# Kernel optimization log

Measured on AMD Instinct MI355X. Metric: run time of the kernel, lower is better.

Reference implementation:

```python
import jax, jax.numpy as jnp
import numpy as np

HEADS = 8  # head_dim = 512 // 8 = 64


def setup_inputs() -> dict:
    key = jax.random.key(0)
    ks = jax.random.split(key, 6)
    B, S, D = 1, 4096, 512
    s = 0.02
    return {
        "hidden_states": jax.random.normal(ks[0], (B, S, D), dtype=jnp.float32),
        "Wq": jax.random.normal(ks[1], (D, D), dtype=jnp.float32) * s,
        "Wk": jax.random.normal(ks[2], (D, D), dtype=jnp.float32) * s,
        "Wv": jax.random.normal(ks[3], (D, D), dtype=jnp.float32) * s,
        "Wo": jax.random.normal(ks[4], (D, D), dtype=jnp.float32) * s,
        "b_out": jnp.zeros((D,), dtype=jnp.float32),
    }


def reference(hidden_states, Wq, Wk, Wv, Wo, b_out):
    B, S, D = hidden_states.shape
    H = HEADS
    hd = D // H
    scale = 1.0 / jnp.sqrt(jnp.asarray(hd, hidden_states.dtype))

    # unfused QKV projections (self-attention, no mask)
    q = hidden_states @ Wq  # [B,S,D]
    k = hidden_states @ Wk
    v = hidden_states @ Wv

    # head_to_batch_dim: [B,S,D] -> [B,H,S,hd]
    def split_heads(t):
        return t.reshape(B, S, H, hd).transpose(0, 2, 1, 3)

    q, k, v = split_heads(q), split_heads(k), split_heads(v)

    # explicit score matrix + softmax (faithful to torch.bmm path)
    scores = jnp.einsum("bhqd,bhkd->bhqk", q, k) * scale  # [B,H,S,S]
    probs = jax.nn.softmax(scores, axis=-1)
    out = jnp.einsum("bhqk,bhkd->bhqd", probs, v)  # [B,H,S,hd]

    # batch_to_head_dim: [B,H,S,hd] -> [B,S,D]
    out = out.transpose(0, 2, 1, 3).reshape(B, S, D)
    # to_out[0] Linear + to_out[1] Dropout (identity at eval)
    return out @ Wo + b_out
```

## Files before the change

kernel.cpp:

```cpp
#include <hip/hip_runtime.h>
#include <hip/hip_bf16.h>

#define S_LEN 4096
#define DMODEL 512
#define NHEADS 8
#define HDIM 64

typedef __hip_bfloat16 bf16;
typedef __attribute__((ext_vector_type(8))) short bf16x8;
typedef __attribute__((ext_vector_type(4))) float f32x4;
typedef __attribute__((ext_vector_type(4))) _Float16 f16x4;
typedef __attribute__((ext_vector_type(8))) _Float16 f16x8;

__device__ __forceinline__ f32x4 mfma16x16x32(bf16x8 a, bf16x8 b, f32x4 c) {
    return __builtin_amdgcn_mfma_f32_16x16x32_bf16(a, b, c, 0, 0, 0);
}
__device__ __forceinline__ f32x4 mfma16x16x16h(f16x4 a, f16x4 b, f32x4 c) {
    return __builtin_amdgcn_mfma_f32_16x16x16f16(a, b, c, 0, 0, 0);
}
__device__ __forceinline__ f16x4 lo4(f16x8 v) { return __builtin_shufflevector(v, v, 0, 1, 2, 3); }
__device__ __forceinline__ f16x4 hi4(f16x8 v) { return __builtin_shufflevector(v, v, 4, 5, 6, 7); }
__device__ __forceinline__ void gload_lds16(const void* g, void* l) {
    __builtin_amdgcn_global_load_lds(
        (const __attribute__((address_space(1))) unsigned int*)g,
        (__attribute__((address_space(3))) unsigned int*)l, 16, 0, 0);
}

__global__ __launch_bounds__(256) void prep(
    const float* __restrict__ X,
    const float* __restrict__ Wq, const float* __restrict__ Wk,
    const float* __restrict__ Wv, const float* __restrict__ Wo,
    bf16* __restrict__ Xb, bf16* __restrict__ Wt)
{
    __shared__ bf16 tile[32][33];
    const int b = blockIdx.x;
    if (b < 1024) {
        int i = (b * 256 + threadIdx.x) * 8;
        float4 a = *(const float4*)(X + i);
        float4 c = *(const float4*)(X + i + 4);
        bf16 tmp[8];
        tmp[0] = __float2bfloat16(a.x); tmp[1] = __float2bfloat16(a.y);
        tmp[2] = __float2bfloat16(a.z); tmp[3] = __float2bfloat16(a.w);
        tmp[4] = __float2bfloat16(c.x); tmp[5] = __float2bfloat16(c.y);
        tmp[6] = __float2bfloat16(c.z); tmp[7] = __float2bfloat16(c.w);
        *(bf16x8*)(Xb + i) = *(bf16x8*)tmp;
    } else {
        const int bb = b - 1024;
        const int z = bb >> 8;
        const int bx = bb & 15, by = (bb >> 4) & 15;
        const float* src = (z == 0) ? Wq : (z == 1) ? Wk : (z == 2) ? Wv : Wo;
        bf16* dst = Wt + (size_t)z * DMODEL * DMODEL;
        const int tx = threadIdx.x & 31, ty = threadIdx.x >> 5;
        const int x = bx * 32 + tx;
        const int y0 = by * 32;
        #pragma unroll
        for (int i = ty; i < 32; i += 8)
            tile[i][tx] = __float2bfloat16(src[(size_t)(y0 + i) * DMODEL + x]);
        __syncthreads();
        const int xo = y0 + tx;
        #pragma unroll
        for (int i = ty; i < 32; i += 8)
            dst[(size_t)(bx * 32 + i) * DMODEL + xo] = tile[tx][i];
    }
}

__global__ __launch_bounds__(256) void gemm_qkv(
    const bf16* __restrict__ A, const bf16* __restrict__ Bt,
    bf16* __restrict__ Qm, bf16* __restrict__ Km, _Float16* __restrict__ Vt)
{
    __shared__ __align__(16) bf16 As[2][64 * 64];
    __shared__ __align__(16) bf16 Bs[2][64 * 64];
    const int m0 = blockIdx.x * 64, n0 = blockIdx.y * 64;
    const int t = threadIdx.x, lane = t & 63, w = t >> 6;
    const int lr = lane & 15, lq = lane >> 4;
    const int swz = (lr & 7) << 4;

    f32x4 acc[4] = {f32x4{0,0,0,0}, f32x4{0,0,0,0}, f32x4{0,0,0,0}, f32x4{0,0,0,0}};

    const int srow = w * 8 + (lane >> 3);
    const int scol = ((lane & 7) ^ (lane >> 3)) * 8;
    const bf16* Ab = A + (size_t)(m0 + srow) * DMODEL + scol;
    const bf16* Bb = Bt + (size_t)(n0 + srow) * DMODEL + scol;
    const int lb = (w * 8) * 64;

#define QKV_STAGE(k0, bsel) do {                                        \
        gload_lds16(Ab + (k0), &As[bsel][lb]);                          \
        gload_lds16(Ab + 32 * DMODEL + (k0), &As[bsel][lb + 32 * 64]);  \
        gload_lds16(Bb + (k0), &Bs[bsel][lb]);                          \
        gload_lds16(Bb + 32 * DMODEL + (k0), &Bs[bsel][lb + 32 * 64]);  \
    } while (0)

    QKV_STAGE(0, 0);
    #pragma unroll
    for (int ks = 0; ks < 8; ++ks) {
        const int cur = ks & 1;
        if (ks < 7) {
            QKV_STAGE((ks + 1) * 64, cur ^ 1);
            asm volatile("s_waitcnt vmcnt(4)" ::: "memory");
        } else {
            asm volatile("s_waitcnt vmcnt(0)" ::: "memory");
        }
        __builtin_amdgcn_s_barrier();
        __builtin_amdgcn_sched_barrier(0);
        const char* Ab8 = (const char*)&As[cur][0];
        const char* Bb8 = (const char*)&Bs[cur][0];
        #pragma unroll
        for (int kc = 0; kc < 2; ++kc) {
            bf16x8 a = *(const bf16x8*)(Ab8 + (w * 16 + lr) * 128 + ((kc * 64 + lq * 16) ^ swz));
            #pragma unroll
            for (int nt = 0; nt < 4; ++nt) {
                bf16x8 b = *(const bf16x8*)(Bb8 + (nt * 16 + lr) * 128 + ((kc * 64 + lq * 16) ^ swz));
                acc[nt] = mfma16x16x32(a, b, acc[nt]);
            }
        }
        asm volatile("s_waitcnt lgkmcnt(0)" ::: "memory");
        __builtin_amdgcn_sched_barrier(0);
        __builtin_amdgcn_s_barrier();
    }
#undef QKV_STAGE

    const int which = n0 >> 9;
    const int nloc = n0 & 511;
    if (which == 0) {
        #pragma unroll
        for (int nt = 0; nt < 4; ++nt)
            #pragma unroll
            for (int r = 0; r < 4; ++r)
                Qm[(size_t)(m0 + w * 16 + lq * 4 + r) * DMODEL + nloc + nt * 16 + lr] =
                    __float2bfloat16(acc[nt][r] * 0.18033688f);
    } else if (which == 1) {
        #pragma unroll
        for (int nt = 0; nt < 4; ++nt)
            #pragma unroll
            for (int r = 0; r < 4; ++r)
                Km[(size_t)(m0 + w * 16 + lq * 4 + r) * DMODEL + nloc + nt * 16 + lr] =
                    __float2bfloat16(acc[nt][r]);
    } else {
        _Float16* tb = (_Float16*)As;
        #pragma unroll
        for (int nt = 0; nt < 4; ++nt)
            #pragma unroll
            for (int r = 0; r < 4; ++r)
                tb[(w * 16 + lq * 4 + r) * 72 + nt * 16 + lr] = (_Float16)acc[nt][r];
        __syncthreads();
        const int c = t >> 2, seg = t & 3;
        _Float16 tmp[16];
        #pragma unroll
        for (int j = 0; j < 16; ++j)
            tmp[j] = tb[(seg * 16 + j) * 72 + c];
        _Float16* vp = Vt + (size_t)(nloc + c) * S_LEN + m0;
        #pragma unroll
        for (int g = 0; g < 4; ++g) {
            f16x4 vv = {tmp[g * 4 + 0], tmp[g * 4 + 1], tmp[g * 4 + 2], tmp[g * 4 + 3]};
            *(f16x4*)(vp + g * 16 + seg * 4) = vv;
        }
    }
}

__global__ __launch_bounds__(256) void gemm_out(
    const bf16* __restrict__ A, const bf16* __restrict__ Bt,
    float* __restrict__ Out, const float* __restrict__ bias)
{
    __shared__ __align__(16) bf16 As[2][64 * 64];
    __shared__ __align__(16) bf16 Bs[2][64 * 64];
    const int m0 = blockIdx.x * 64, n0 = blockIdx.y * 64;
    const int t = threadIdx.x, lane = t & 63, w = t >> 6;
    const int lr = lane & 15, lq = lane >> 4;
    const int swz = (lr & 7) << 4;

    f32x4 acc[4] = {f32x4{0,0,0,0}, f32x4{0,0,0,0}, f32x4{0,0,0,0}, f32x4{0,0,0,0}};

    const int srow = w * 8 + (lane >> 3);
    const int scol = ((lane & 7) ^ (lane >> 3)) * 8;
    const bf16* Ab = A + (size_t)(m0 + srow) * DMODEL + scol;
    const bf16* Bb = Bt + (size_t)(n0 + srow) * DMODEL + scol;
    const int lb = (w * 8) * 64;

#define OUT_STAGE(k0, bsel) do {                                        \
        gload_lds16(Ab + (k0), &As[bsel][lb]);                          \
        gload_lds16(Ab + 32 * DMODEL + (k0), &As[bsel][lb + 32 * 64]);  \
        gload_lds16(Bb + (k0), &Bs[bsel][lb]);                          \
        gload_lds16(Bb + 32 * DMODEL + (k0), &Bs[bsel][lb + 32 * 64]);  \
    } while (0)

    OUT_STAGE(0, 0);
    #pragma unroll
    for (int ks = 0; ks < 8; ++ks) {
        const int cur = ks & 1;
        if (ks < 7) {
            OUT_STAGE((ks + 1) * 64, cur ^ 1);
            asm volatile("s_waitcnt vmcnt(4)" ::: "memory");
        } else {
            asm volatile("s_waitcnt vmcnt(0)" ::: "memory");
        }
        __builtin_amdgcn_s_barrier();
        __builtin_amdgcn_sched_barrier(0);
        const char* Ab8 = (const char*)&As[cur][0];
        const char* Bb8 = (const char*)&Bs[cur][0];
        #pragma unroll
        for (int kc = 0; kc < 2; ++kc) {
            bf16x8 a = *(const bf16x8*)(Ab8 + (w * 16 + lr) * 128 + ((kc * 64 + lq * 16) ^ swz));
            #pragma unroll
            for (int nt = 0; nt < 4; ++nt) {
                bf16x8 b = *(const bf16x8*)(Bb8 + (nt * 16 + lr) * 128 + ((kc * 64 + lq * 16) ^ swz));
                acc[nt] = mfma16x16x32(a, b, acc[nt]);
            }
        }
        asm volatile("s_waitcnt lgkmcnt(0)" ::: "memory");
        __builtin_amdgcn_sched_barrier(0);
        __builtin_amdgcn_s_barrier();
    }
#undef OUT_STAGE

    #pragma unroll
    for (int nt = 0; nt < 4; ++nt)
        #pragma unroll
        for (int r = 0; r < 4; ++r)
            Out[(size_t)(m0 + w * 16 + lq * 4 + r) * DMODEL + n0 + nt * 16 + lr] =
                acc[nt][r] + bias[n0 + nt * 16 + lr];
}

__global__ __launch_bounds__(256, 2) void attn_kernel(
    const bf16* __restrict__ Q, const bf16* __restrict__ Kmat,
    const _Float16* __restrict__ Vt, bf16* __restrict__ Oout)
{
    __shared__ __align__(16) char smem[65536];

    const int h = blockIdx.x, qb = blockIdx.y;
    const int t = threadIdx.x, lane = t & 63, w = t >> 6;
    const int lr = lane & 15, lq = lane >> 4;
    const int q0 = qb * 64;

    char* myK = smem + w * 16384;
    char* myV = myK + 8192;

    const int sr = lane >> 3;
    const int scc = (lane & 7) ^ sr;
    const bf16*     gK = Kmat + (size_t)sr * DMODEL + h * HDIM + scc * 8;
    const _Float16* gV = Vt + (size_t)(h * HDIM + sr) * S_LEN + scc * 8;

    bf16x8 qf[4][2];
    #pragma unroll
    for (int qt = 0; qt < 4; ++qt) {
        const bf16* qp = Q + (size_t)(q0 + qt * 16 + lr) * DMODEL + h * HDIM + lq * 8;
        qf[qt][0] = *(const bf16x8*)qp;
        qf[qt][1] = *(const bf16x8*)(qp + 32);
    }

    f32x4 oacc[4][4];
    #pragma unroll
    for (int i = 0; i < 4; ++i)
        #pragma unroll
        for (int j = 0; j < 4; ++j) oacc[i][j] = f32x4{0, 0, 0, 0};
    float lsum[4] = {0, 0, 0, 0};

    #pragma unroll
    for (int i = 0; i < 8; ++i) {
        gload_lds16(gK + (size_t)(w * 64 + i * 8) * DMODEL, myK + i * 1024);
        gload_lds16(gV + (size_t)(i * 8) * S_LEN + w * 64, myV + i * 1024);
    }

    const int swz = (lr & 7) << 4;

    for (int kt = w; kt < S_LEN / 64; kt += 4) {
        asm volatile("s_waitcnt vmcnt(0)" ::: "memory");

        bf16x8 kf[4][2];
        #pragma unroll
        for (int mt = 0; mt < 4; ++mt) {
            const char* kr = myK + (mt * 16 + lr) * 128;
            kf[mt][0] = *(const bf16x8*)(kr + ((lq * 16) ^ swz));
            kf[mt][1] = *(const bf16x8*)(kr + ((64 + lq * 16) ^ swz));
        }
        f16x8 vA[4], vB[4];
        #pragma unroll
        for (int ht = 0; ht < 4; ++ht) {
            const char* vr = myV + (ht * 16 + lr) * 128;
            vA[ht] = *(const f16x8*)(vr + ((lq * 32) ^ swz));
            vB[ht] = *(const f16x8*)(vr + ((lq * 32 + 16) ^ swz));
        }
        asm volatile("s_waitcnt lgkmcnt(0)" ::: "memory");
        __builtin_amdgcn_sched_barrier(0);

        const int ktn = kt + 4;
        if (ktn < S_LEN / 64) {
            #pragma unroll
            for (int i = 0; i < 8; ++i) {
                gload_lds16(gK + (size_t)(ktn * 64 + i * 8) * DMODEL, myK + i * 1024);
                gload_lds16(gV + (size_t)(i * 8) * S_LEN + ktn * 64, myV + i * 1024);
            }
        }

        __builtin_amdgcn_s_setprio(1);
        f16x4 pf[4][4];
        #pragma unroll
        for (int qt = 0; qt < 4; ++qt) {
            f32x4 st[4];
            #pragma unroll
            for (int mt = 0; mt < 4; ++mt) {
                f32x4 z = {0, 0, 0, 0};
                z = mfma16x16x32(kf[mt][0], qf[qt][0], z);
                z = mfma16x16x32(kf[mt][1], qf[qt][1], z);
                st[mt] = z;
            }
            #pragma unroll
            for (int mt = 0; mt < 4; ++mt)
                #pragma unroll
                for (int r = 0; r < 4; ++r) {
                    float p = __builtin_amdgcn_exp2f(st[mt][r]);
                    lsum[qt] += p;
                    pf[qt][mt][r] = (_Float16)p;
                }
        }
        #pragma unroll
        for (int qt = 0; qt < 4; ++qt)
            #pragma unroll
            for (int ht = 0; ht < 4; ++ht) {
                oacc[qt][ht] = mfma16x16x16h(pf[qt][0], lo4(vA[ht]), oacc[qt][ht]);
                oacc[qt][ht] = mfma16x16x16h(pf[qt][1], hi4(vA[ht]), oacc[qt][ht]);
                oacc[qt][ht] = mfma16x16x16h(pf[qt][2], lo4(vB[ht]), oacc[qt][ht]);
                oacc[qt][ht] = mfma16x16x16h(pf[qt][3], hi4(vB[ht]), oacc[qt][ht]);
            }
        __builtin_amdgcn_s_setprio(0);
    }

    __syncthreads();
    float (*obuf)[3][4][64][4] = (float(*)[3][4][64][4])smem;
    float (*lbuf)[4][16]       = (float(*)[4][16])(smem + 49152);

    #pragma unroll
    for (int qt = 0; qt < 4; ++qt) {
        if (qt != w) {
            int j = qt - (qt > w ? 1 : 0);
            #pragma unroll
            for (int ht = 0; ht < 4; ++ht)
                *(f32x4*)&obuf[w][j][ht][lane][0] = oacc[qt][ht];
        }
    }
    #pragma unroll
    for (int qt = 0; qt < 4; ++qt) {
        float s = lsum[qt];
        s += __shfl_xor(s, 16);
        s += __shfl_xor(s, 32);
        if (lq == 0) lbuf[w][qt][lr] = s;
    }
    __syncthreads();

    f32x4 osum[4];
    #pragma unroll
    for (int qt = 0; qt < 4; ++qt)
        if (qt == w) {
            #pragma unroll
            for (int ht = 0; ht < 4; ++ht) osum[ht] = oacc[qt][ht];
        }
    #pragma unroll
    for (int w2 = 0; w2 < 4; ++w2) {
        if (w2 == w) continue;
        int j = w - (w > w2 ? 1 : 0);
        #pragma unroll
        for (int ht = 0; ht < 4; ++ht)
            osum[ht] += *(const f32x4*)&obuf[w2][j][ht][lane][0];
    }
    float linv[4];
    #pragma unroll
    for (int r = 0; r < 4; ++r) {
        int rr = lq * 4 + r;
        linv[r] = 1.0f / (lbuf[0][w][rr] + lbuf[1][w][rr] + lbuf[2][w][rr] + lbuf[3][w][rr]);
    }
    #pragma unroll
    for (int r = 0; r < 4; ++r) {
        int row = q0 + w * 16 + lq * 4 + r;
        #pragma unroll
        for (int ht = 0; ht < 4; ++ht)
            Oout[(size_t)row * DMODEL + h * HDIM + ht * 16 + lr] =
                __float2bfloat16(osum[ht][r] * linv[r]);
    }
}

extern "C" void kernel_launch(void* const* d_in, const int* in_sizes, int n_in,
                              void* d_out, int out_size, void* d_ws, size_t ws_size,
                              hipStream_t stream) {
    const float* X  = (const float*)d_in[0];
    const float* Wq = (const float*)d_in[1];
    const float* Wk = (const float*)d_in[2];
    const float* Wv = (const float*)d_in[3];
    const float* Wo = (const float*)d_in[4];
    const float* bo = (const float*)d_in[5];
    float* out = (float*)d_out;

    char* ws = (char*)d_ws;
    bf16* Wt = (bf16*)ws;
    bf16* Xb = (bf16*)(ws + (size_t)4 * DMODEL * DMODEL * 2);
    bf16* Qm = Xb + (size_t)S_LEN * DMODEL;
    bf16* Km = Qm + (size_t)S_LEN * DMODEL;
    _Float16* Vt = (_Float16*)(Km + (size_t)S_LEN * DMODEL);
    bf16* AO = (bf16*)(Vt + (size_t)S_LEN * DMODEL);

    bf16* Wot = Wt + (size_t)3 * DMODEL * DMODEL;

    prep<<<2048, 256, 0, stream>>>(X, Wq, Wk, Wv, Wo, Xb, Wt);

    gemm_qkv<<<dim3(S_LEN / 64, 3 * DMODEL / 64), 256, 0, stream>>>(
        Xb, Wt, Qm, Km, Vt);

    attn_kernel<<<dim3(NHEADS, S_LEN / 64), 256, 0, stream>>>(Qm, Km, Vt, AO);

    gemm_out<<<dim3(S_LEN / 64, DMODEL / 64), 256, 0, stream>>>(AO, Wot, out, bo);
}
```

Baseline: 134.7 us.

## Fuse QKV tiles per block, use 16x16x32 f16 MFMA, vectorize epilogues

The QKV GEMM now computes Q, K and V tiles for the same rows in one block, reusing the A tile across three weight matrices and cutting the grid to a third. Epilogues for Q/K and the output GEMM are staged through shared memory so global stores become 16-byte row-contiguous writes. In attention, the four 16x16x16 f16 MFMAs per tile are replaced by two 16x16x32 f16 MFMAs, and probabilities are packed with cvt_pkrtz conversions. The trade-offs are more LDS per QKV block (64KB) with lower occupancy, and round-toward-zero rounding of the probabilities.

```diff
diff --git a/kernel.cpp b/kernel.cpp
--- a/kernel.cpp
+++ b/kernel.cpp
@@ -9,17 +9,16 @@
 typedef __hip_bfloat16 bf16;
 typedef __attribute__((ext_vector_type(8))) short bf16x8;
 typedef __attribute__((ext_vector_type(4))) float f32x4;
+typedef __attribute__((ext_vector_type(2))) _Float16 f16x2;
 typedef __attribute__((ext_vector_type(4))) _Float16 f16x4;
 typedef __attribute__((ext_vector_type(8))) _Float16 f16x8;
 
 __device__ __forceinline__ f32x4 mfma16x16x32(bf16x8 a, bf16x8 b, f32x4 c) {
     return __builtin_amdgcn_mfma_f32_16x16x32_bf16(a, b, c, 0, 0, 0);
 }
-__device__ __forceinline__ f32x4 mfma16x16x16h(f16x4 a, f16x4 b, f32x4 c) {
-    return __builtin_amdgcn_mfma_f32_16x16x16f16(a, b, c, 0, 0, 0);
-}
-__device__ __forceinline__ f16x4 lo4(f16x8 v) { return __builtin_shufflevector(v, v, 0, 1, 2, 3); }
-__device__ __forceinline__ f16x4 hi4(f16x8 v) { return __builtin_shufflevector(v, v, 4, 5, 6, 7); }
+__device__ __forceinline__ f32x4 mfma16x16x32h(f16x8 a, f16x8 b, f32x4 c) {
+    return __builtin_amdgcn_mfma_f32_16x16x32_f16(a, b, c, 0, 0, 0);
+}
 __device__ __forceinline__ void gload_lds16(const void* g, void* l) {
     __builtin_amdgcn_global_load_lds(
         (const __attribute__((address_space(1))) unsigned int*)g,
@@ -68,26 +67,33 @@
     const bf16* __restrict__ A, const bf16* __restrict__ Bt,
     bf16* __restrict__ Qm, bf16* __restrict__ Km, _Float16* __restrict__ Vt)
 {
-    __shared__ __align__(16) bf16 As[2][64 * 64];
-    __shared__ __align__(16) bf16 Bs[2][64 * 64];
+    __shared__ __align__(16) char smem[65536];
     const int m0 = blockIdx.x * 64, n0 = blockIdx.y * 64;
     const int t = threadIdx.x, lane = t & 63, w = t >> 6;
     const int lr = lane & 15, lq = lane >> 4;
     const int swz = (lr & 7) << 4;
 
-    f32x4 acc[4] = {f32x4{0,0,0,0}, f32x4{0,0,0,0}, f32x4{0,0,0,0}, f32x4{0,0,0,0}};
+    f32x4 acc[3][4];
+    #pragma unroll
+    for (int i = 0; i < 3; ++i)
+        #pragma unroll
+        for (int n = 0; n < 4; ++n) acc[i][n] = f32x4{0, 0, 0, 0};
 
     const int srow = w * 8 + (lane >> 3);
     const int scol = ((lane & 7) ^ (lane >> 3)) * 8;
     const bf16* Ab = A + (size_t)(m0 + srow) * DMODEL + scol;
     const bf16* Bb = Bt + (size_t)(n0 + srow) * DMODEL + scol;
-    const int lb = (w * 8) * 64;
-
-#define QKV_STAGE(k0, bsel) do {                                        \
-        gload_lds16(Ab + (k0), &As[bsel][lb]);                          \
-        gload_lds16(Ab + 32 * DMODEL + (k0), &As[bsel][lb + 32 * 64]);  \
-        gload_lds16(Bb + (k0), &Bs[bsel][lb]);                          \
-        gload_lds16(Bb + 32 * DMODEL + (k0), &Bs[bsel][lb + 32 * 64]);  \
+
+#define QKV_STAGE(k0, b) do {                                                  \
+        char* ad = smem + (b) * 8192 + w * 1024;                               \
+        gload_lds16(Ab + (k0), ad);                                            \
+        gload_lds16(Ab + 32 * DMODEL + (k0), ad + 4096);                       \
+        _Pragma("unroll")                                                      \
+        for (int mat = 0; mat < 3; ++mat) {                                    \
+            char* bd = smem + 16384 + ((b) * 3 + mat) * 8192 + w * 1024;       \
+            gload_lds16(Bb + mat * DMODEL * DMODEL + (k0), bd);                \
+            gload_lds16(Bb + mat * DMODEL * DMODEL + 32 * DMODEL + (k0), bd + 4096); \
+        }                                                                      \
     } while (0)
 
     QKV_STAGE(0, 0);
@@ -96,22 +102,24 @@
         const int cur = ks & 1;
         if (ks < 7) {
             QKV_STAGE((ks + 1) * 64, cur ^ 1);
-            asm volatile("s_waitcnt vmcnt(4)" ::: "memory");
+            asm volatile("s_waitcnt vmcnt(8)" ::: "memory");
         } else {
             asm volatile("s_waitcnt vmcnt(0)" ::: "memory");
         }
         __builtin_amdgcn_s_barrier();
         __builtin_amdgcn_sched_barrier(0);
-        const char* Ab8 = (const char*)&As[cur][0];
-        const char* Bb8 = (const char*)&Bs[cur][0];
         #pragma unroll
         for (int kc = 0; kc < 2; ++kc) {
-            bf16x8 a = *(const bf16x8*)(Ab8 + (w * 16 + lr) * 128 + ((kc * 64 + lq * 16) ^ swz));
-            #pragma unroll
-            for (int nt = 0; nt < 4; ++nt) {
-                bf16x8 b = *(const bf16x8*)(Bb8 + (nt * 16 + lr) * 128 + ((kc * 64 + lq * 16) ^ swz));
-                acc[nt] = mfma16x16x32(a, b, acc[nt]);
-            }
+            const int co = (kc * 64 + lq * 16) ^ swz;
+            bf16x8 a = *(const bf16x8*)(smem + cur * 8192 + (w * 16 + lr) * 128 + co);
+            #pragma unroll
+            for (int mat = 0; mat < 3; ++mat)
+                #pragma unroll
+                for (int nt = 0; nt < 4; ++nt) {
+                    bf16x8 b = *(const bf16x8*)(smem + 16384 + (cur * 3 + mat) * 8192 +
+                                                (nt * 16 + lr) * 128 + co);
+                    acc[mat][nt] = mfma16x16x32(a, b, acc[mat][nt]);
+                }
         }
         asm volatile("s_waitcnt lgkmcnt(0)" ::: "memory");
         __builtin_amdgcn_sched_barrier(0);
@@ -119,36 +127,34 @@
     }
 #undef QKV_STAGE
 
-    const int which = n0 >> 9;
-    const int nloc = n0 & 511;
-    if (which == 0) {
-        #pragma unroll
-        for (int nt = 0; nt < 4; ++nt)
-            #pragma unroll
-            for (int r = 0; r < 4; ++r)
-                Qm[(size_t)(m0 + w * 16 + lq * 4 + r) * DMODEL + nloc + nt * 16 + lr] =
-                    __float2bfloat16(acc[nt][r] * 0.18033688f);
-    } else if (which == 1) {
-        #pragma unroll
-        for (int nt = 0; nt < 4; ++nt)
-            #pragma unroll
-            for (int r = 0; r < 4; ++r)
-                Km[(size_t)(m0 + w * 16 + lq * 4 + r) * DMODEL + nloc + nt * 16 + lr] =
-                    __float2bfloat16(acc[nt][r]);
-    } else {
-        _Float16* tb = (_Float16*)As;
-        #pragma unroll
-        for (int nt = 0; nt < 4; ++nt)
-            #pragma unroll
-            for (int r = 0; r < 4; ++r)
-                tb[(w * 16 + lq * 4 + r) * 72 + nt * 16 + lr] = (_Float16)acc[nt][r];
-        __syncthreads();
+    bf16*     tbq = (bf16*)smem;
+    bf16*     tbk = (bf16*)(smem + 9216);
+    _Float16* tbv = (_Float16*)(smem + 18432);
+    #pragma unroll
+    for (int nt = 0; nt < 4; ++nt)
+        #pragma unroll
+        for (int r = 0; r < 4; ++r) {
+            int row = w * 16 + lq * 4 + r, col = nt * 16 + lr;
+            tbq[row * 72 + col] = __float2bfloat16(acc[0][nt][r] * 0.18033688f);
+            tbk[row * 72 + col] = __float2bfloat16(acc[1][nt][r]);
+            tbv[row * 72 + col] = (_Float16)acc[2][nt][r];
+        }
+    __syncthreads();
+    #pragma unroll
+    for (int pass = 0; pass < 2; ++pass) {
+        const int m = pass * 32 + (t >> 3), c0 = (t & 7) * 8;
+        *(bf16x8*)(Qm + (size_t)(m0 + m) * DMODEL + n0 + c0) =
+            *(const bf16x8*)(tbq + m * 72 + c0);
+        *(bf16x8*)(Km + (size_t)(m0 + m) * DMODEL + n0 + c0) =
+            *(const bf16x8*)(tbk + m * 72 + c0);
+    }
+    {
         const int c = t >> 2, seg = t & 3;
         _Float16 tmp[16];
         #pragma unroll
         for (int j = 0; j < 16; ++j)
-            tmp[j] = tb[(seg * 16 + j) * 72 + c];
-        _Float16* vp = Vt + (size_t)(nloc + c) * S_LEN + m0;
+            tmp[j] = tbv[(seg * 16 + j) * 72 + c];
+        _Float16* vp = Vt + (size_t)(n0 + c) * S_LEN + m0;
         #pragma unroll
         for (int g = 0; g < 4; ++g) {
             f16x4 vv = {tmp[g * 4 + 0], tmp[g * 4 + 1], tmp[g * 4 + 2], tmp[g * 4 + 3]};
@@ -161,8 +167,7 @@
     const bf16* __restrict__ A, const bf16* __restrict__ Bt,
     float* __restrict__ Out, const float* __restrict__ bias)
 {
-    __shared__ __align__(16) bf16 As[2][64 * 64];
-    __shared__ __align__(16) bf16 Bs[2][64 * 64];
+    __shared__ __align__(16) char smem[32768];
     const int m0 = blockIdx.x * 64, n0 = blockIdx.y * 64;
     const int t = threadIdx.x, lane = t & 63, w = t >> 6;
     const int lr = lane & 15, lq = lane >> 4;
@@ -174,13 +179,14 @@
     const int scol = ((lane & 7) ^ (lane >> 3)) * 8;
     const bf16* Ab = A + (size_t)(m0 + srow) * DMODEL + scol;
     const bf16* Bb = Bt + (size_t)(n0 + srow) * DMODEL + scol;
-    const int lb = (w * 8) * 64;
-
-#define OUT_STAGE(k0, bsel) do {                                        \
-        gload_lds16(Ab + (k0), &As[bsel][lb]);                          \
-        gload_lds16(Ab + 32 * DMODEL + (k0), &As[bsel][lb + 32 * 64]);  \
-        gload_lds16(Bb + (k0), &Bs[bsel][lb]);                          \
-        gload_lds16(Bb + 32 * DMODEL + (k0), &Bs[bsel][lb + 32 * 64]);  \
+
+#define OUT_STAGE(k0, b) do {                                           \
+        char* ad = smem + (b) * 8192 + w * 1024;                        \
+        char* bd = smem + 16384 + (b) * 8192 + w * 1024;                \
+        gload_lds16(Ab + (k0), ad);                                     \
+        gload_lds16(Ab + 32 * DMODEL + (k0), ad + 4096);                \
+        gload_lds16(Bb + (k0), bd);                                     \
+        gload_lds16(Bb + 32 * DMODEL + (k0), bd + 4096);                \
     } while (0)
 
     OUT_STAGE(0, 0);
@@ -195,14 +201,13 @@
         }
         __builtin_amdgcn_s_barrier();
         __builtin_amdgcn_sched_barrier(0);
-        const char* Ab8 = (const char*)&As[cur][0];
-        const char* Bb8 = (const char*)&Bs[cur][0];
         #pragma unroll
         for (int kc = 0; kc < 2; ++kc) {
-            bf16x8 a = *(const bf16x8*)(Ab8 + (w * 16 + lr) * 128 + ((kc * 64 + lq * 16) ^ swz));
+            const int co = (kc * 64 + lq * 16) ^ swz;
+            bf16x8 a = *(const bf16x8*)(smem + cur * 8192 + (w * 16 + lr) * 128 + co);
             #pragma unroll
             for (int nt = 0; nt < 4; ++nt) {
-                bf16x8 b = *(const bf16x8*)(Bb8 + (nt * 16 + lr) * 128 + ((kc * 64 + lq * 16) ^ swz));
+                bf16x8 b = *(const bf16x8*)(smem + 16384 + cur * 8192 + (nt * 16 + lr) * 128 + co);
                 acc[nt] = mfma16x16x32(a, b, acc[nt]);
             }
         }
@@ -212,12 +217,23 @@
     }
 #undef OUT_STAGE
 
-    #pragma unroll
-    for (int nt = 0; nt < 4; ++nt)
+    float* tb = (float*)smem;
+    #pragma unroll
+    for (int nt = 0; nt < 4; ++nt) {
+        const float bv = bias[n0 + nt * 16 + lr];
         #pragma unroll
         for (int r = 0; r < 4; ++r)
-            Out[(size_t)(m0 + w * 16 + lq * 4 + r) * DMODEL + n0 + nt * 16 + lr] =
-                acc[nt][r] + bias[n0 + nt * 16 + lr];
+            tb[(w * 16 + lq * 4 + r) * 68 + nt * 16 + lr] = acc[nt][r] + bv;
+    }
+    __syncthreads();
+    #pragma unroll
+    for (int pass = 0; pass < 2; ++pass) {
+        const int m = pass * 32 + (t >> 3), c0 = (t & 7) * 8;
+        float4 v0 = *(const float4*)(tb + m * 68 + c0);
+        float4 v1 = *(const float4*)(tb + m * 68 + c0 + 4);
+        *(float4*)(Out + (size_t)(m0 + m) * DMODEL + n0 + c0) = v0;
+        *(float4*)(Out + (size_t)(m0 + m) * DMODEL + n0 + c0 + 4) = v1;
+    }
 }
 
 __global__ __launch_bounds__(256, 2) void attn_kernel(
@@ -304,23 +320,27 @@
                 st[mt] = z;
             }
             #pragma unroll
-            for (int mt = 0; mt < 4; ++mt)
-                #pragma unroll
-                for (int r = 0; r < 4; ++r) {
-                    float p = __builtin_amdgcn_exp2f(st[mt][r]);
-                    lsum[qt] += p;
-                    pf[qt][mt][r] = (_Float16)p;
-                }
-        }
-        #pragma unroll
-        for (int qt = 0; qt < 4; ++qt)
+            for (int mt = 0; mt < 4; ++mt) {
+                float p0 = __builtin_amdgcn_exp2f(st[mt][0]);
+                float p1 = __builtin_amdgcn_exp2f(st[mt][1]);
+                float p2 = __builtin_amdgcn_exp2f(st[mt][2]);
+                float p3 = __builtin_amdgcn_exp2f(st[mt][3]);
+                lsum[qt] += (p0 + p1) + (p2 + p3);
+                f16x2 c01 = __builtin_bit_cast(f16x2, __builtin_amdgcn_cvt_pkrtz(p0, p1));
+                f16x2 c23 = __builtin_bit_cast(f16x2, __builtin_amdgcn_cvt_pkrtz(p2, p3));
+                pf[qt][mt] = __builtin_shufflevector(c01, c23, 0, 1, 2, 3);
+            }
+        }
+        #pragma unroll
+        for (int qt = 0; qt < 4; ++qt) {
+            f16x8 pp01 = __builtin_shufflevector(pf[qt][0], pf[qt][1], 0, 1, 2, 3, 4, 5, 6, 7);
+            f16x8 pp23 = __builtin_shufflevector(pf[qt][2], pf[qt][3], 0, 1, 2, 3, 4, 5, 6, 7);
             #pragma unroll
             for (int ht = 0; ht < 4; ++ht) {
-                oacc[qt][ht] = mfma16x16x16h(pf[qt][0], lo4(vA[ht]), oacc[qt][ht]);
-                oacc[qt][ht] = mfma16x16x16h(pf[qt][1], hi4(vA[ht]), oacc[qt][ht]);
-                oacc[qt][ht] = mfma16x16x16h(pf[qt][2], lo4(vB[ht]), oacc[qt][ht]);
-                oacc[qt][ht] = mfma16x16x16h(pf[qt][3], hi4(vB[ht]), oacc[qt][ht]);
+                oacc[qt][ht] = mfma16x16x32h(pp01, vA[ht], oacc[qt][ht]);
+                oacc[qt][ht] = mfma16x16x32h(pp23, vB[ht], oacc[qt][ht]);
             }
+        }
         __builtin_amdgcn_s_setprio(0);
     }
 
@@ -400,7 +420,7 @@
 
     prep<<<2048, 256, 0, stream>>>(X, Wq, Wk, Wv, Wo, Xb, Wt);
 
-    gemm_qkv<<<dim3(S_LEN / 64, 3 * DMODEL / 64), 256, 0, stream>>>(
+    gemm_qkv<<<dim3(S_LEN / 64, DMODEL / 64), 256, 0, stream>>>(
         Xb, Wt, Qm, Km, Vt);
 
     attn_kernel<<<dim3(NHEADS, S_LEN / 64), 256, 0, stream>>>(Qm, Km, Vt, AO);
```

After: 128.3 us. -4.8%, faster.
